# Kernel optimization log

Measured on AMD Instinct MI355X. Metric: run time of the kernel, lower is better.

Reference implementation:

```python
import jax, jax.numpy as jnp
import numpy as np

B, L, N, H, HU = 512, 16, 10000, 128, 128

def _rn(k, shape, s=0.05):
    return jax.random.normal(k, shape, jnp.float32) * s

def setup_inputs():
    ks = jax.random.split(jax.random.key(0), 26)
    return dict(
        x=jax.random.normal(ks[0], (B, 2), jnp.float32),
        t0_res=jax.random.normal(ks[1], (B, 1), jnp.float32),
        node_inputs=jax.random.normal(ks[2], (B, 2 * L, N), jnp.float32),
        tau_inputs=jax.random.normal(ks[3], (B, L, 1), jnp.float32),
        end=jax.random.normal(ks[4], (B, 2), jnp.float32),
        coords=jax.random.normal(ks[5], (B, 2 * L, 2), jnp.float32),
        Wx1=_rn(ks[6], (1, 2)), Wx2=_rn(ks[7], (H, 1)), bx2=_rn(ks[8], (H,)),
        Wres=_rn(ks[9], (H, 1)), bres=_rn(ks[10], (H,)),
        Wnode=_rn(ks[11], (H, N)),
        Wtau=_rn(ks[12], (H, 1)), btau=_rn(ks[13], (H,)),
        Wend1=_rn(ks[14], (1, 2)), Wend2=_rn(ks[15], (H, 1)), bend2=_rn(ks[16], (H,)),
        Wcoord=_rn(ks[17], (H, 2)),
        lstm_Wih=_rn(ks[18], (7, 4 * H, H)), lstm_Whh=_rn(ks[19], (7, 4 * H, H)),
        lstm_bih=_rn(ks[20], (7, 4 * H)), lstm_bhh=_rn(ks[21], (7, 4 * H)),
        head_W1=_rn(ks[22], (7, HU, H)), head_b1=_rn(ks[23], (7, HU)),
        head_W2=_rn(ks[24], (7, 1, HU)), head_b2=_rn(ks[25], (7, 1)),
    )

def _lstm_last(s, Wih, Whh, bih, bhh):
    # s: [T, B, H] (time-first, like torch LSTM default). PyTorch gate order: i, f, g, o.
    h0 = jnp.zeros((s.shape[1], Whh.shape[1]), s.dtype)
    def step(carry, xt):
        h, c = carry
        g = xt @ Wih.T + h @ Whh.T + (bih + bhh)
        i, f, gg, o = jnp.split(g, 4, axis=-1)
        c = jax.nn.sigmoid(f) * c + jax.nn.sigmoid(i) * jnp.tanh(gg)
        h = jax.nn.sigmoid(o) * jnp.tanh(c)
        return (h, c), None
    (h, _), _ = jax.lax.scan(step, (h0, h0), s)
    return h  # last output == last hidden state

def _forward(x, t0_res, node_inputs, tau_inputs, end, coords,
             Wx1, Wx2, bx2, Wres, bres, Wnode, Wtau, btau,
             Wend1, Wend2, bend2, Wcoord,
             lstm_Wih, lstm_Whh, lstm_bih, lstm_bhh,
             head_W1, head_b1, head_W2, head_b2):
    xh = jnp.tanh((x @ Wx1.T) @ Wx2.T + bx2)        # [B,H]
    t0h = jnp.tanh(t0_res @ Wres.T + bres)          # [B,H]
    nodeh = node_inputs @ Wnode.T                   # [B,2L,H] (dominant memory-bound GEMM)
    tauh = jnp.tanh(tau_inputs @ Wtau.T + btau)     # [B,L,H]
    endh = (end @ Wend1.T) @ Wend2.T + bend2        # [B,H]
    coordh = coords @ Wcoord.T                      # [B,2L,H]
    ne, no = nodeh[:, 0::2], nodeh[:, 1::2]         # even/odd walk nodes [B,L,H]
    ce, co = coordh[:, 0::2], coordh[:, 1::2]
    def interleave(parts):  # k x [B,L,H] -> time-first [k*L, B, H], per-step order preserved
        s = jnp.stack(parts, axis=2)
        return jnp.swapaxes(s.reshape(s.shape[0], -1, s.shape[-1]), 0, 1)
    pre = jnp.stack([xh, t0h], axis=0)  # [2,B,H]
    suf = endh[None]                    # [1,B,H]
    seqs = [
        jnp.concatenate([pre, interleave([tauh, ne, ce, no, co]), suf], 0),  # all        T=5L+3
        jnp.concatenate([pre, interleave([tauh]), suf], 0),                  # time       T=L+3
        jnp.swapaxes(nodeh, 0, 1),                                           # node       T=2L
        jnp.swapaxes(coordh, 0, 1),                                          # coord      T=2L
        jnp.concatenate([pre, interleave([tauh, ne, no]), suf], 0),          # node_time  T=3L+3
        interleave([ne, ce, no, co]),                                        # node_coord T=4L
        jnp.concatenate([pre, interleave([tauh, ce, co]), suf], 0),          # time_coord T=3L+3
    ]
    outs = []
    for k, s in enumerate(seqs):
        h = _lstm_last(s, lstm_Wih[k], lstm_Whh[k], lstm_bih[k], lstm_bhh[k])
        outs.append(jnp.tanh(h @ head_W1[k].T + head_b1[k]) @ head_W2[k].T + head_b2[k])
    return tuple(outs)  # matches torch return order: all, time, node, coord, node_time, node_coord, time_coord

def reference(x, t0_res, node_inputs, tau_inputs, end, coords,
              Wx1, Wx2, bx2, Wres, bres, Wnode, Wtau, btau,
              Wend1, Wend2, bend2, Wcoord,
              lstm_Wih, lstm_Whh, lstm_bih, lstm_bhh,
              head_W1, head_b1, head_W2, head_b2):
    return _forward(x, t0_res, node_inputs, tau_inputs, end, coords,
                    Wx1, Wx2, bx2, Wres, bres, Wnode, Wtau, btau,
                    Wend1, Wend2, bend2, Wcoord,
                    lstm_Wih, lstm_Whh, lstm_bih, lstm_bhh,
                    head_W1, head_b1, head_W2, head_b2)
```

## Files before the change

### kernel.cpp

```cpp
#include <hip/hip_runtime.h>
#include <hip/hip_fp16.h>

typedef _Float16 f16;
typedef _Float16 f16x8 __attribute__((ext_vector_type(8)));
typedef float f32x4 __attribute__((ext_vector_type(4)));

#define NB 512
#define NL 16
#define NK 10000
#define NH 128
#define NSF 316
#define NT 79

__device__ __forceinline__ float fast_exp2(float x) {
#if __has_builtin(__builtin_amdgcn_exp2f)
  return __builtin_amdgcn_exp2f(x);
#else
  return exp2f(x);
#endif
}
__device__ __forceinline__ float fast_rcp(float x) {
#if __has_builtin(__builtin_amdgcn_rcpf)
  return __builtin_amdgcn_rcpf(x);
#else
  return 1.f / x;
#endif
}
__device__ __forceinline__ float sigf(float x) {
  return fast_rcp(1.f + fast_exp2(-1.44269504f * x));
}
__device__ __forceinline__ float tanh_fast(float x) {
  return 2.f * fast_rcp(1.f + fast_exp2(-2.88539008f * x)) - 1.f;
}

__global__ void prep_kernel(
    const float* __restrict__ x, const float* __restrict__ t0,
    const float* __restrict__ tau, const float* __restrict__ endi,
    const float* __restrict__ coords,
    const float* __restrict__ Wx1, const float* __restrict__ Wx2,
    const float* __restrict__ bx2, const float* __restrict__ Wres,
    const float* __restrict__ bres, const float* __restrict__ Wnode,
    const float* __restrict__ Wtau, const float* __restrict__ btau,
    const float* __restrict__ Wend1, const float* __restrict__ Wend2,
    const float* __restrict__ bend2, const float* __restrict__ Wcoord,
    const float* __restrict__ Wih, const float* __restrict__ Whh,
    const float* __restrict__ bih, const float* __restrict__ bhh,
    f16* __restrict__ xh, f16* __restrict__ t0h, f16* __restrict__ endh,
    f16* __restrict__ tauh, f16* __restrict__ coordh, f16* __restrict__ Wf,
    f16* __restrict__ Wih16, f16* __restrict__ Whh16, float* __restrict__ bsum) {
  const int tid0 = blockIdx.x * blockDim.x + threadIdx.x;
  const int stride = gridDim.x * blockDim.x;

  const int nWf = NSF * 4096;
  const int nW = 7 * 512 * NH;
  const int nb = 7 * 512;
  const int nxh = NB * NH;
  const int ntau = NB * NL * NH;
  const int nco = NB * 2 * NL * NH;

  for (int i = tid0; i < nWf; i += stride) {
    const int s = i >> 12, r = i & 4095;
    const int nt = r >> 9, l2 = r & 511;
    const int lane = l2 >> 3, e = l2 & 7;
    const int kg = lane >> 4, lr = lane & 15;
    const int col = nt * 16 + lr;
    const int k = s * 32 + kg * 8 + e;
    Wf[i] = (k < NK) ? (f16)Wnode[(size_t)col * NK + k] : (f16)0.f;
  }
  for (int i = tid0; i < nW; i += stride) {
    Wih16[i] = (f16)Wih[i];
    Whh16[i] = (f16)Whh[i];
  }
  for (int i = tid0; i < nb; i += stride) bsum[i] = bih[i] + bhh[i];
  for (int i = tid0; i < nxh; i += stride) {
    const int b = i >> 7, h = i & 127;
    const float s = x[2 * b] * Wx1[0] + x[2 * b + 1] * Wx1[1];
    xh[i] = (f16)tanhf(s * Wx2[h] + bx2[h]);
    t0h[i] = (f16)tanhf(t0[b] * Wres[h] + bres[h]);
    const float e = endi[2 * b] * Wend1[0] + endi[2 * b + 1] * Wend1[1];
    endh[i] = (f16)(e * Wend2[h] + bend2[h]);
  }
  for (int i = tid0; i < ntau; i += stride) {
    const int h = i & 127, bl = i >> 7;
    tauh[i] = (f16)tanhf(tau[bl] * Wtau[h] + btau[h]);
  }
  for (int i = tid0; i < nco; i += stride) {
    const int h = i & 127, br = i >> 7;
    coordh[i] = (f16)(coords[2 * br] * Wcoord[2 * h] +
                      coords[2 * br + 1] * Wcoord[2 * h + 1]);
  }
}

__global__ __launch_bounds__(512, 2) void node_gemm(const float* __restrict__ A,
                                                    const f16* __restrict__ Wf,
                                                    f16* __restrict__ Cn) {
  __shared__ char lds[4][32768];
  const int tid = threadIdx.x;
  const int w = tid >> 6, l = tid & 63;
  const int lr = l & 15, kg = l >> 4;
  const int r0 = blockIdx.x * 64;
  char* lds0 = &lds[0][0];

  const char* ap[4];
  int bnd[4], wdo[4];
#pragma unroll
  for (int i = 0; i < 4; i++) {
    const int row = w * 8 + i * 2 + (l >> 5);
    const int off = (l & 31) * 16;
    ap[i] = (const char*)A + (size_t)(r0 + row) * 40000 + off;
    bnd[i] = 39984 - off;
    wdo[i] = row * 512 + (off ^ ((row & 7) << 4));
  }

  const int kw = w & 1, cp = w >> 1;
  int rdoA[4][2][2];
#pragma unroll
  for (int rg = 0; rg < 4; rg++) {
    const int row = rg * 16 + lr;
    const int sw = (row & 7) << 4;
#pragma unroll
    for (int ks = 0; ks < 2; ks++)
#pragma unroll
      for (int h = 0; h < 2; h++)
        rdoA[rg][ks][h] =
            row * 512 + ((kw * 256 + ks * 128 + kg * 32 + h * 16) ^ sw);
  }

  f32x4 acc[4][2];
#pragma unroll
  for (int rg = 0; rg < 4; rg++)
#pragma unroll
    for (int j = 0; j < 2; j++) {
      f32x4 z = {0.f, 0.f, 0.f, 0.f};
      acc[rg][j] = z;
    }

  auto loadA = [&](int t, f32x4 (&r)[4]) {
    const int tb = t * 512;
#pragma unroll
    for (int i = 0; i < 4; i++) {
      const int off = tb < bnd[i] ? tb : bnd[i];
      r[i] = __builtin_nontemporal_load((const f32x4*)(ap[i] + off));
    }
  };

  auto dswrite = [&](int t, const f32x4 (&r)[4]) {
    char* db = lds0 + (t & 3) * 32768;
#pragma unroll
    for (int i = 0; i < 4; i++) *(f32x4*)(db + wdo[i]) = r[i];
  };

  auto loadB = [&](int t, f16x8 (&B)[2][2]) {
    const f16* bp = Wf + (size_t)(4 * t + 2 * kw) * 4096 + cp * 1024 + l * 8;
#pragma unroll
    for (int j = 0; j < 2; j++)
#pragma unroll
      for (int ks = 0; ks < 2; ks++)
        B[j][ks] = *(const f16x8*)(bp + (size_t)ks * 4096 + j * 512);
  };

  auto compute = [&](int t, const f16x8 (&B)[2][2]) {
    const char* cb = lds0 + (t & 3) * 32768;
#pragma unroll
    for (int ks = 0; ks < 2; ks++)
#pragma unroll
      for (int rg = 0; rg < 4; rg++) {
        const f32x4 a0 = *(const f32x4*)(cb + rdoA[rg][ks][0]);
        const f32x4 a1 = *(const f32x4*)(cb + rdoA[rg][ks][1]);
        f16x8 af;
        af[0] = (f16)a0[0]; af[1] = (f16)a0[1];
        af[2] = (f16)a0[2]; af[3] = (f16)a0[3];
        af[4] = (f16)a1[0]; af[5] = (f16)a1[1];
        af[6] = (f16)a1[2]; af[7] = (f16)a1[3];
#pragma unroll
        for (int j = 0; j < 2; j++)
          acc[rg][j] = __builtin_amdgcn_mfma_f32_16x16x32_f16(
              af, B[j][ks], acc[rg][j], 0, 0, 0);
      }
  };

  f32x4 RA[4], RB[4];
  f16x8 BA[2][2], BB[2][2];

  loadA(0, RA);
  asm volatile("s_waitcnt vmcnt(0)" ::: "memory");
  dswrite(0, RA);
  loadA(1, RB);
  loadB(0, BA);
  asm volatile("s_waitcnt lgkmcnt(0)" ::: "memory");
  __builtin_amdgcn_s_barrier();

  for (int e = 0; e + 1 < NT; e += 2) {
    asm volatile("s_waitcnt vmcnt(0)" ::: "memory");
    dswrite(e + 1, RB);
    loadA(e + 2, RA);
    loadB(e + 1, BB);
    asm volatile("s_waitcnt lgkmcnt(0)" ::: "memory");
    __builtin_amdgcn_s_barrier();
    compute(e, BA);
    asm volatile("s_waitcnt vmcnt(0)" ::: "memory");
    dswrite(e + 2, RA);
    if (e + 3 < NT) loadA(e + 3, RB);
    loadB(e + 2, BA);
    asm volatile("s_waitcnt lgkmcnt(0)" ::: "memory");
    __builtin_amdgcn_s_barrier();
    compute(e + 1, BB);
  }
  compute(NT - 1, BA);

  __syncthreads();
  if (kw == 1) {
#pragma unroll
    for (int rg = 0; rg < 4; rg++)
#pragma unroll
      for (int j = 0; j < 2; j++) {
        const int tl = cp * 8 + rg * 2 + j;
        *(f32x4*)(lds0 + tl * 1024 + l * 16) = acc[rg][j];
      }
  }
  __syncthreads();
  if (kw == 0) {
#pragma unroll
    for (int rg = 0; rg < 4; rg++)
#pragma unroll
      for (int j = 0; j < 2; j++) {
        const int tl = cp * 8 + rg * 2 + j;
        const f32x4 p = *(const f32x4*)(lds0 + tl * 1024 + l * 16);
        const f32x4 s = acc[rg][j] + p;
        f16* crow =
            Cn + (size_t)(r0 + rg * 16 + kg * 4) * NH + cp * 32 + j * 16 + lr;
#pragma unroll
        for (int jr = 0; jr < 4; jr++) crow[(size_t)jr * NH] = (f16)s[jr];
      }
  }
}

__global__ __launch_bounds__(512, 2) void lstm_run(
    const f16* __restrict__ xh, const f16* __restrict__ t0h,
    const f16* __restrict__ endh, const f16* __restrict__ tauh,
    const f16* __restrict__ nodeh, const f16* __restrict__ coordh,
    const f16* __restrict__ Wih16, const f16* __restrict__ Whh16,
    const float* __restrict__ bsum, const float* __restrict__ hW1,
    const float* __restrict__ hb1, const float* __restrict__ hW2,
    const float* __restrict__ hb2, float* __restrict__ out) {
  __shared__ f16 hbuf[2][16 * NH];
  __shared__ float hu[16 * NH];

  const int k = blockIdx.x >> 5;
  const int b0 = (blockIdx.x & 31) << 4;
  const int w = threadIdx.x >> 6;
  const int l = threadIdx.x & 63;
  const int lr = l & 15, kg = l >> 4;

  int len;
  switch (k) {
    case 0: len = 83; break;
    case 1: len = 19; break;
    case 2: len = 32; break;
    case 3: len = 32; break;
    case 4: len = 51; break;
    case 5: len = 64; break;
    default: len = 51; break;
  }

  auto xptr = [&](int t) -> const f16* {
    const f16* cb; int bstr, idx;
    if (k == 2) { cb = nodeh; bstr = 32 * NH; idx = t; }
    else if (k == 3) { cb = coordh; bstr = 32 * NH; idx = t; }
    else if (k == 5) {
      const int q = t >> 2, r = t & 3;
      cb = (r == 0 || r == 2) ? nodeh : coordh;
      bstr = 32 * NH;
      idx = 2 * q + ((r >= 2) ? 1 : 0);
    } else {
      if (t == 0) { cb = xh; bstr = NH; idx = 0; }
      else if (t == 1) { cb = t0h; bstr = NH; idx = 0; }
      else if (t == len - 1) { cb = endh; bstr = NH; idx = 0; }
      else {
        const int u = t - 2;
        if (k == 0) {
          const int q = u / 5, r = u - 5 * q;
          if (r == 0) { cb = tauh; bstr = 16 * NH; idx = q; }
          else if (r == 1) { cb = nodeh; bstr = 32 * NH; idx = 2 * q; }
          else if (r == 2) { cb = coordh; bstr = 32 * NH; idx = 2 * q; }
          else if (r == 3) { cb = nodeh; bstr = 32 * NH; idx = 2 * q + 1; }
          else { cb = coordh; bstr = 32 * NH; idx = 2 * q + 1; }
        } else if (k == 1) { cb = tauh; bstr = 16 * NH; idx = u; }
        else if (k == 4) {
          const int q = u / 3, r = u - 3 * q;
          if (r == 0) { cb = tauh; bstr = 16 * NH; idx = q; }
          else { cb = nodeh; bstr = 32 * NH; idx = 2 * q + (r - 1); }
        } else {
          const int q = u / 3, r = u - 3 * q;
          if (r == 0) { cb = tauh; bstr = 16 * NH; idx = q; }
          else { cb = coordh; bstr = 32 * NH; idx = 2 * q + (r - 1); }
        }
      }
    }
    return cb + (size_t)(b0 + lr) * bstr + idx * NH + kg * 8;
  };

  f16x8 Wh[4][4], Wi[4][4];
  float bias[4];
  {
    const f16* whb = Whh16 + (size_t)k * 512 * NH;
    const f16* wib = Wih16 + (size_t)k * 512 * NH;
#pragma unroll
    for (int g = 0; g < 4; g++) {
      const int col = g * 128 + w * 16 + lr;
      bias[g] = bsum[k * 512 + col];
#pragma unroll
      for (int kc = 0; kc < 4; kc++) {
        Wh[kc][g] = *(const f16x8*)(whb + (size_t)col * NH + kc * 32 + kg * 8);
        Wi[kc][g] = *(const f16x8*)(wib + (size_t)col * NH + kc * 32 + kg * 8);
      }
    }
  }

  char* lds0 = (char*)&hbuf[0][0];
  *(unsigned long long*)(lds0 + threadIdx.x * 8) = 0ull;
  __syncthreads();

  float c[4] = {0, 0, 0, 0};

  int rdo[4];
#pragma unroll
  for (int kc = 0; kc < 4; kc++) {
    const int colb = (kc * 32 + kg * 8) * 2;
    rdo[kc] = lr * 256 + (colb ^ ((lr & 7) << 4));
  }
  int wro[4];
#pragma unroll
  for (int jr = 0; jr < 4; jr++) {
    const int hrow = kg * 4 + jr;
    const int hcol = w * 16 + lr;
    wro[jr] = hrow * 256 + ((hcol * 2) ^ ((hrow & 7) << 4));
  }

  f16x8 axc[4];
  {
    const f16* xp = xptr(0);
#pragma unroll
    for (int kc = 0; kc < 4; kc++) axc[kc] = *(const f16x8*)(xp + kc * 32);
  }

  int cur = 0;
  for (int t = 0; t < len; t++) {
    char* rb = lds0 + cur * 4096;
    f16x8 ah[4];
#pragma unroll
    for (int kc = 0; kc < 4; kc++) ah[kc] = *(const f16x8*)(rb + rdo[kc]);

    f16x8 axn[4];
    if (t + 1 < len) {
      const f16* xp = xptr(t + 1);
#pragma unroll
      for (int kc = 0; kc < 4; kc++) axn[kc] = *(const f16x8*)(xp + kc * 32);
    }

    f32x4 acc[4];
#pragma unroll
    for (int g = 0; g < 4; g++) {
      f32x4 binit = {bias[g], bias[g], bias[g], bias[g]};
      acc[g] = binit;
    }
#pragma unroll
    for (int kc = 0; kc < 4; kc++)
#pragma unroll
      for (int g = 0; g < 4; g++)
        acc[g] = __builtin_amdgcn_mfma_f32_16x16x32_f16(axc[kc], Wi[kc][g], acc[g], 0, 0, 0);
#pragma unroll
    for (int kc = 0; kc < 4; kc++)
#pragma unroll
      for (int g = 0; g < 4; g++)
        acc[g] = __builtin_amdgcn_mfma_f32_16x16x32_f16(ah[kc], Wh[kc][g], acc[g], 0, 0, 0);

    char* wb = lds0 + (cur ^ 1) * 4096;
#pragma unroll
    for (int jr = 0; jr < 4; jr++) {
      const float iv = acc[0][jr];
      const float fv = acc[1][jr];
      const float gv = acc[2][jr];
      const float ov = acc[3][jr];
      const float cn = sigf(fv) * c[jr] + sigf(iv) * tanh_fast(gv);
      c[jr] = cn;
      const float hn = sigf(ov) * tanh_fast(cn);
      *(f16*)(wb + wro[jr]) = (f16)hn;
    }
    __syncthreads();
#pragma unroll
    for (int kc = 0; kc < 4; kc++) axc[kc] = axn[kc];
    cur ^= 1;
  }

  {
    char* rb = lds0 + cur * 4096;
    f16x8 ah[4];
#pragma unroll
    for (int kc = 0; kc < 4; kc++) ah[kc] = *(const f16x8*)(rb + rdo[kc]);
    const float* W1 = hW1 + (size_t)k * NH * NH;
    const int col = w * 16 + lr;
    f32x4 hacc;
    {
      const float b1 = hb1[k * NH + col];
      f32x4 binit = {b1, b1, b1, b1};
      hacc = binit;
    }
#pragma unroll
    for (int kc = 0; kc < 4; kc++) {
      const float* wrow = W1 + (size_t)col * NH + kc * 32 + kg * 8;
      const f32x4 w0 = *(const f32x4*)(wrow);
      const f32x4 w1 = *(const f32x4*)(wrow + 4);
      f16x8 wv;
      wv[0] = (f16)w0[0]; wv[1] = (f16)w0[1]; wv[2] = (f16)w0[2]; wv[3] = (f16)w0[3];
      wv[4] = (f16)w1[0]; wv[5] = (f16)w1[1]; wv[6] = (f16)w1[2]; wv[7] = (f16)w1[3];
      hacc = __builtin_amdgcn_mfma_f32_16x16x32_f16(ah[kc], wv, hacc, 0, 0, 0);
    }
#pragma unroll
    for (int jr = 0; jr < 4; jr++)
      hu[(kg * 4 + jr) * NH + col] = tanh_fast(hacc[jr]);
  }
  __syncthreads();
  if (w == 0) {
    const int b = l >> 2, part = l & 3;
    const float* W2 = hW2 + (size_t)k * NH;
    float s = 0.f;
#pragma unroll
    for (int j = 0; j < 32; j++)
      s += hu[b * NH + part * 32 + j] * W2[part * 32 + j];
    s += __shfl_xor(s, 1);
    s += __shfl_xor(s, 2);
    if (part == 0) out[k * NB + b0 + b] = s + hb2[k];
  }
}

extern "C" void kernel_launch(void* const* d_in, const int* in_sizes, int n_in,
                              void* d_out, int out_size, void* d_ws, size_t ws_size,
                              hipStream_t stream) {
  (void)in_sizes; (void)n_in; (void)out_size; (void)ws_size;
  const float* x = (const float*)d_in[0];
  const float* t0 = (const float*)d_in[1];
  const float* node = (const float*)d_in[2];
  const float* tau = (const float*)d_in[3];
  const float* endi = (const float*)d_in[4];
  const float* coords = (const float*)d_in[5];
  const float* Wx1 = (const float*)d_in[6];
  const float* Wx2 = (const float*)d_in[7];
  const float* bx2 = (const float*)d_in[8];
  const float* Wres = (const float*)d_in[9];
  const float* bres = (const float*)d_in[10];
  const float* Wnode = (const float*)d_in[11];
  const float* Wtau = (const float*)d_in[12];
  const float* btau = (const float*)d_in[13];
  const float* Wend1 = (const float*)d_in[14];
  const float* Wend2 = (const float*)d_in[15];
  const float* bend2 = (const float*)d_in[16];
  const float* Wcoord = (const float*)d_in[17];
  const float* Wih = (const float*)d_in[18];
  const float* Whh = (const float*)d_in[19];
  const float* bih = (const float*)d_in[20];
  const float* bhh = (const float*)d_in[21];
  const float* hW1 = (const float*)d_in[22];
  const float* hb1 = (const float*)d_in[23];
  const float* hW2 = (const float*)d_in[24];
  const float* hb2 = (const float*)d_in[25];

  char* ws = (char*)d_ws;
  f16* xh = (f16*)ws;      ws += (size_t)NB * NH * 2;
  f16* t0h = (f16*)ws;     ws += (size_t)NB * NH * 2;
  f16* endh = (f16*)ws;    ws += (size_t)NB * NH * 2;
  f16* tauh = (f16*)ws;    ws += (size_t)NB * NL * NH * 2;
  f16* nodeh = (f16*)ws;   ws += (size_t)NB * 2 * NL * NH * 2;
  f16* coordh = (f16*)ws;  ws += (size_t)NB * 2 * NL * NH * 2;
  f16* Wf = (f16*)ws;      ws += (size_t)NSF * 4096 * 2;
  f16* Wih16 = (f16*)ws;   ws += (size_t)7 * 512 * NH * 2;
  f16* Whh16 = (f16*)ws;   ws += (size_t)7 * 512 * NH * 2;
  float* bsum = (float*)ws;

  prep_kernel<<<1024, 256, 0, stream>>>(
      x, t0, tau, endi, coords, Wx1, Wx2, bx2, Wres, bres, Wnode, Wtau, btau,
      Wend1, Wend2, bend2, Wcoord, Wih, Whh, bih, bhh,
      xh, t0h, endh, tauh, coordh, Wf, Wih16, Whh16, bsum);
  node_gemm<<<256, 512, 0, stream>>>(node, Wf, nodeh);
  lstm_run<<<224, 512, 0, stream>>>(xh, t0h, endh, tauh, nodeh, coordh,
                                    Wih16, Whh16, bsum, hW1, hb1, hW2, hb2,
                                    (float*)d_out);
}
```

Before: 250.1 us.

## Deepen A-tile prefetch pipeline with partial vmcnt waits and temporal loads

Restructures the main GEMM loop so two A tiles are in flight and each iteration waits only for the older loads (vmcnt(4)) before writing to LDS, instead of draining all outstanding global loads. B loads are issued before A loads so the counter-based wait ordering works. It also replaces nontemporal loads of the node inputs with normal loads. The goal is more overlap of HBM latency with MFMA compute, at the cost of correctness relying on load issue order matching the vmcnt counts.

```diff
diff --git a/kernel.cpp b/kernel.cpp
--- a/kernel.cpp
+++ b/kernel.cpp
@@ -140,7 +140,7 @@
 #pragma unroll
     for (int i = 0; i < 4; i++) {
       const int off = tb < bnd[i] ? tb : bnd[i];
-      r[i] = __builtin_nontemporal_load((const f32x4*)(ap[i] + off));
+      r[i] = *(const f32x4*)(ap[i] + off);
     }
   };
 
@@ -179,34 +179,34 @@
       }
   };
 
-  f32x4 RA[4], RB[4];
-  f16x8 BA[2][2], BB[2][2];
-
-  loadA(0, RA);
+  f32x4 RA0[4], RA1[4];
+  f16x8 B0[2][2], B1[2][2];
+
+  loadA(0, RA0);
+  loadB(0, B0);
+  loadA(1, RA1);
+
+  for (int e = 0; e + 1 < NT; e += 2) {
+    asm volatile("s_waitcnt vmcnt(4)" ::: "memory");
+    dswrite(e, RA0);
+    loadB(e + 1, B1);
+    loadA(e + 2, RA0);
+    asm volatile("s_waitcnt lgkmcnt(0)" ::: "memory");
+    __builtin_amdgcn_s_barrier();
+    compute(e, B0);
+    asm volatile("s_waitcnt vmcnt(4)" ::: "memory");
+    dswrite(e + 1, RA1);
+    loadB(e + 2, B0);
+    if (e + 3 < NT) loadA(e + 3, RA1);
+    asm volatile("s_waitcnt lgkmcnt(0)" ::: "memory");
+    __builtin_amdgcn_s_barrier();
+    compute(e + 1, B1);
+  }
   asm volatile("s_waitcnt vmcnt(0)" ::: "memory");
-  dswrite(0, RA);
-  loadA(1, RB);
-  loadB(0, BA);
+  dswrite(NT - 1, RA0);
   asm volatile("s_waitcnt lgkmcnt(0)" ::: "memory");
   __builtin_amdgcn_s_barrier();
-
-  for (int e = 0; e + 1 < NT; e += 2) {
-    asm volatile("s_waitcnt vmcnt(0)" ::: "memory");
-    dswrite(e + 1, RB);
-    loadA(e + 2, RA);
-    loadB(e + 1, BB);
-    asm volatile("s_waitcnt lgkmcnt(0)" ::: "memory");
-    __builtin_amdgcn_s_barrier();
-    compute(e, BA);
-    asm volatile("s_waitcnt vmcnt(0)" ::: "memory");
-    dswrite(e + 2, RA);
-    if (e + 3 < NT) loadA(e + 3, RB);
-    loadB(e + 2, BA);
-    asm volatile("s_waitcnt lgkmcnt(0)" ::: "memory");
-    __builtin_amdgcn_s_barrier();
-    compute(e + 1, BB);
-  }
-  compute(NT - 1, BA);
+  compute(NT - 1, B0);
 
   __syncthreads();
   if (kw == 1) {
```

Result: slower. 259.0 us (+3.6%).
